# Kernel optimization log

Hardware: AMD Instinct MI355X
Metric: run time of the kernel (lower is better)

Reference implementation:

```python
import jax, jax.numpy as jnp
import numpy as np

# Config constants (from model_cfg)
X_RANGE = (0.0, 70.4)
Y_RANGE = (-40.0, 40.0)
Z_RANGE = (-3.0, 1.0)
RES = 0.2
Z_RES = 0.8
B, C, RH, RW = 2, 64, 64, 2048
W = int((Y_RANGE[1] - Y_RANGE[0]) / RES)   # 400
H = int((X_RANGE[1] - X_RANGE[0]) / RES)   # 352
D = int((Z_RANGE[1] - Z_RANGE[0]) / Z_RES) # 5


def setup_inputs() -> dict:
    key = jax.random.key(0)
    k1, k2, k3, k4 = jax.random.split(key, 4)
    range_res = jax.random.normal(k1, (B, C, RH, RW), dtype=jnp.float32)
    # realistic lidar xyz: x forward, y lateral, z height (slightly wider than
    # the crop ranges so clamping / z-dropping paths are exercised)
    x = jax.random.uniform(k2, (B, 1, RH, RW), minval=-5.0, maxval=75.0)
    y = jax.random.uniform(k3, (B, 1, RH, RW), minval=-45.0, maxval=45.0)
    z = jax.random.uniform(k4, (B, 1, RH, RW), minval=-3.5, maxval=1.5)
    rangemap_xyz = jnp.concatenate([x, y, z], axis=1).astype(jnp.float32)
    return {"range_res": range_res, "rangemap_xyz": rangemap_xyz, "batch_size": B}


def reference(range_res, rangemap_xyz, batch_size):
    b, c, rh, rw = range_res.shape
    n = rh * rw
    pts = rangemap_xyz.reshape(b, 3, n)            # [B,3,N]
    xp, yp, zp = pts[:, 0], pts[:, 1], pts[:, 2]   # [B,N] each
    feat = range_res.reshape(b, c, n).transpose(0, 2, 1)  # [B,N,C]

    # torch .long() truncates toward zero, as does astype(int32)
    x_img = (-yp / RES).astype(jnp.int32) - int(np.floor(Y_RANGE[0] / RES))
    y_img = (-xp / RES).astype(jnp.int32) + int(np.floor(X_RANGE[1] / RES))
    x_img = jnp.clip(x_img, 0, W - 1)
    y_img = jnp.clip(y_img, 0, H - 1)

    # height-bin index; points outside [z0, z1) are dropped (never scattered)
    zbin = jnp.floor((zp - Z_RANGE[0]) / Z_RES).astype(jnp.int32)
    valid = (zp >= Z_RANGE[0]) & (zp < Z_RANGE[1])
    zbin = jnp.where(valid, zbin, D)  # D is out-of-bounds -> mode='drop'

    # im is flipped along both spatial dims after the scatter; equivalent to
    # scattering at flipped indices.
    xf = (W - 1) - x_img
    yf = (H - 1) - y_img

    bidx = jnp.arange(b, dtype=jnp.int32)[:, None]  # [B,1] broadcast over N
    bev = jnp.zeros((b, D, W, H, c), dtype=range_res.dtype)
    bev = bev.at[bidx, zbin, xf, yf].set(feat, mode="drop")

    # original: bev [b,w,h,c,d] -> permute(0,3,4,1,2) = [b,c,d,w,h]
    # ours is [b,d,w,h,c] -> [b,c,d,w,h]
    return bev.transpose(0, 4, 1, 2, 3)
```

## Files before the change

### kernel.cpp

```cpp
#include <hip/hip_runtime.h>


namespace {

typedef float v4f __attribute__((ext_vector_type(4)));

constexpr int Wg    = 400;
constexpr int Hg    = 352;
constexpr int Dg    = 5;
constexpr int NCELL = Dg * Wg * Hg;
constexpr int NPTS  = 64 * 2048;
constexpr int CC    = 64;
constexpr int BB    = 2;
constexpr int CPB   = 1024;
constexpr int NCHUNK = (NCELL + CPB - 1) / CPB;

__global__ void scatter_winner_k(const float* __restrict__ xyz,
                                 int* __restrict__ winner) {
    int idx = blockIdx.x * blockDim.x + threadIdx.x;
    if (idx >= BB * NPTS) return;
    int b = idx >> 17;
    int i = idx & (NPTS - 1);
    const float* base = xyz + (size_t)b * 3 * NPTS;
    float xp = base[i];
    float yp = base[NPTS + i];
    float zp = base[2 * NPTS + i];
    if (!(zp >= -3.0f && zp < 1.0f)) return;
    int zbin  = (int)floorf((zp + 3.0f) / 0.8f);
    int x_img = (int)(-yp / 0.2f) + 200;
    int y_img = (int)(-xp / 0.2f) + 352;
    x_img = min(max(x_img, 0), Wg - 1);
    y_img = min(max(y_img, 0), Hg - 1);
    int xf = (Wg - 1) - x_img;
    int yf = (Hg - 1) - y_img;
    int cell = (zbin * Wg + xf) * Hg + yf;
    atomicMax(winner + b * NCELL + cell, i);
}

__global__ __launch_bounds__(256) void write_out_k(
        const float* __restrict__ feat,
        const int*   __restrict__ winner,
        float*       __restrict__ out) {
    int blk   = blockIdx.x;
    int b     = blk / NCHUNK;
    int chunk = blk - b * NCHUNK;
    int cell0 = chunk * CPB + (int)threadIdx.x * 4;
    if (cell0 >= NCELL) return;

    const int4 w4 = *reinterpret_cast<const int4*>(winner + b * NCELL + cell0);
    const bool v0 = w4.x >= 0, v1 = w4.y >= 0, v2 = w4.z >= 0, v3 = w4.w >= 0;
    const int  i0 = max(w4.x, 0), i1 = max(w4.y, 0);
    const int  i2 = max(w4.z, 0), i3 = max(w4.w, 0);

    const float* fb = feat + (size_t)b * CC * NPTS;
    float*       ob = out  + (size_t)b * CC * NCELL + cell0;

#pragma unroll 2
    for (int c = 0; c < CC; ++c) {
        const float* frow = fb + (size_t)c * NPTS;
        float g0 = frow[i0], g1 = frow[i1], g2 = frow[i2], g3 = frow[i3];
        v4f v;
        v.x = v0 ? g0 : 0.0f;
        v.y = v1 ? g1 : 0.0f;
        v.z = v2 ? g2 : 0.0f;
        v.w = v3 ? g3 : 0.0f;
        __builtin_nontemporal_store(v, reinterpret_cast<v4f*>(ob + (size_t)c * NCELL));
    }
}

}

extern "C" void kernel_launch(void* const* d_in, const int* in_sizes, int n_in,
                              void* d_out, int out_size, void* d_ws, size_t ws_size,
                              hipStream_t stream) {
    const float* range_res = (const float*)d_in[0];
    const float* xyz       = (const float*)d_in[1];
    float* out             = (float*)d_out;
    int* winner            = (int*)d_ws;

    (void)hipMemsetAsync(winner, 0xFF, (size_t)BB * NCELL * sizeof(int), stream);

    {
        int total = BB * NPTS;
        scatter_winner_k<<<(total + 255) / 256, 256, 0, stream>>>(xyz, winner);
    }
    {
        int blocks = BB * NCHUNK;
        write_out_k<<<blocks, 256, 0, stream>>>(range_res, winner, out);
    }
}
```

Measured before the change: 555.7 us.

## Restructure output writer to per-channel row blocks with contiguous cell streaming

The write-out kernel previously assigned each block a chunk of cells and looped over all 64 channels, gathering from 64 different feature rows. Now each block owns one (batch, channel) pair and one eighth of the cells. It re-reads winner indices and gathers from a single 512 KB feature row that can stay in cache. Block ids are interleaved so that 8 channels sharing the same winner slice run together. The cost is that the winner array is read once per channel instead of once, which adds extra winner traffic.

```diff
diff --git a/kernel.cpp b/kernel.cpp
--- a/kernel.cpp
+++ b/kernel.cpp
@@ -12,8 +12,9 @@
 constexpr int NPTS  = 64 * 2048;
 constexpr int CC    = 64;
 constexpr int BB    = 2;
-constexpr int CPB   = 1024;
-constexpr int NCHUNK = (NCELL + CPB - 1) / CPB;
+constexpr int Q     = 8;
+constexpr int CPC   = NCELL / Q;
+constexpr int VPC   = CPC / 4;
 
 __global__ void scatter_winner_k(const float* __restrict__ xyz,
                                  int* __restrict__ winner) {
@@ -41,30 +42,30 @@
         const float* __restrict__ feat,
         const int*   __restrict__ winner,
         float*       __restrict__ out) {
-    int blk   = blockIdx.x;
-    int b     = blk / NCHUNK;
-    int chunk = blk - b * NCHUNK;
-    int cell0 = chunk * CPB + (int)threadIdx.x * 4;
-    if (cell0 >= NCELL) return;
+    int blk  = blockIdx.x;
+    int x    = blk & 7;
+    int q    = (blk >> 3) & 7;
+    int bchi = blk >> 6;
+    int bc   = bchi * 8 + x;
+    int b    = bc >> 6;
 
-    const int4 w4 = *reinterpret_cast<const int4*>(winner + b * NCELL + cell0);
-    const bool v0 = w4.x >= 0, v1 = w4.y >= 0, v2 = w4.z >= 0, v3 = w4.w >= 0;
-    const int  i0 = max(w4.x, 0), i1 = max(w4.y, 0);
-    const int  i2 = max(w4.z, 0), i3 = max(w4.w, 0);
-
-    const float* fb = feat + (size_t)b * CC * NPTS;
-    float*       ob = out  + (size_t)b * CC * NCELL + cell0;
+    const int*   wbase = winner + b * NCELL + q * CPC;
+    const float* frow  = feat + (size_t)bc * NPTS;
+    float*       obase = out + (size_t)bc * NCELL + q * CPC;
 
 #pragma unroll 2
-    for (int c = 0; c < CC; ++c) {
-        const float* frow = fb + (size_t)c * NPTS;
-        float g0 = frow[i0], g1 = frow[i1], g2 = frow[i2], g3 = frow[i3];
+    for (int i = threadIdx.x; i < VPC; i += 256) {
+        const int4 w4 = reinterpret_cast<const int4*>(wbase)[i];
+        float g0 = frow[max(w4.x, 0)];
+        float g1 = frow[max(w4.y, 0)];
+        float g2 = frow[max(w4.z, 0)];
+        float g3 = frow[max(w4.w, 0)];
         v4f v;
-        v.x = v0 ? g0 : 0.0f;
-        v.y = v1 ? g1 : 0.0f;
-        v.z = v2 ? g2 : 0.0f;
-        v.w = v3 ? g3 : 0.0f;
-        __builtin_nontemporal_store(v, reinterpret_cast<v4f*>(ob + (size_t)c * NCELL));
+        v.x = (w4.x >= 0) ? g0 : 0.0f;
+        v.y = (w4.y >= 0) ? g1 : 0.0f;
+        v.z = (w4.z >= 0) ? g2 : 0.0f;
+        v.w = (w4.w >= 0) ? g3 : 0.0f;
+        __builtin_nontemporal_store(v, reinterpret_cast<v4f*>(obase) + i);
     }
 }
 
@@ -85,7 +86,7 @@
         scatter_winner_k<<<(total + 255) / 256, 256, 0, stream>>>(xyz, winner);
     }
     {
-        int blocks = BB * NCHUNK;
+        int blocks = BB * CC * Q;
         write_out_k<<<blocks, 256, 0, stream>>>(range_res, winner, out);
     }
 }
```

New measurement: 488.9 us. -12.0%, faster.

## Transpose features to point-major layout and stage BEV writes through shared memory

Applied to the files above, without the earlier changes.

Adds a pre-pass that transposes features from channel-major to point-major so each winning point's 64 channels are read contiguously. The output kernel gathers per-cell channel vectors into a shared tile, then writes channel-major output with coalesced stores. The goal is to replace 64 scattered gathers per cell with contiguous reads. In exchange it adds an extra full read and write of the feature tensor and drops the vectorized 4-wide stores.

```diff
diff --git a/kernel.cpp b/kernel.cpp
--- a/kernel.cpp
+++ b/kernel.cpp
@@ -2,8 +2,6 @@
 
 
 namespace {
-
-typedef float v4f __attribute__((ext_vector_type(4)));
 
 constexpr int Wg    = 400;
 constexpr int Hg    = 352;
@@ -12,8 +10,8 @@
 constexpr int NPTS  = 64 * 2048;
 constexpr int CC    = 64;
 constexpr int BB    = 2;
-constexpr int CPB   = 1024;
-constexpr int NCHUNK = (NCELL + CPB - 1) / CPB;
+constexpr int GRP   = 64;
+constexpr int NGRP  = NCELL / GRP;
 
 __global__ void scatter_winner_k(const float* __restrict__ xyz,
                                  int* __restrict__ winner) {
@@ -37,34 +35,62 @@
     atomicMax(winner + b * NCELL + cell, i);
 }
 
-__global__ __launch_bounds__(256) void write_out_k(
-        const float* __restrict__ feat,
-        const int*   __restrict__ winner,
-        float*       __restrict__ out) {
+__global__ __launch_bounds__(256) void transpose_k(const float* __restrict__ feat,
+                                                   float* __restrict__ featT) {
+    __shared__ float tile[64][65];
+    int blk = blockIdx.x;
+    int b   = blk >> 11;
+    int n0  = (blk & 2047) * 64;
+    const float* fb = feat  + (size_t)b * CC * NPTS;
+    float*       tb = featT + (size_t)b * NPTS * CC;
+    int t = threadIdx.x;
+#pragma unroll
+    for (int k = 0; k < 16; ++k) {
+        int j = k * 256 + t;
+        int c = j >> 6, nn = j & 63;
+        tile[c][nn] = fb[(size_t)c * NPTS + n0 + nn];
+    }
+    __syncthreads();
+#pragma unroll
+    for (int k = 0; k < 16; ++k) {
+        int j = k * 256 + t;
+        int nn = j >> 6, c = j & 63;
+        tb[(size_t)(n0 + nn) * CC + c] = tile[c][nn];
+    }
+}
+
+__global__ __launch_bounds__(256) void bev_write_k(const float* __restrict__ featT,
+                                                   const int*   __restrict__ winner,
+                                                   float*       __restrict__ out) {
+    __shared__ float tile[GRP][65];
+    __shared__ int   wins[GRP];
     int blk   = blockIdx.x;
-    int b     = blk / NCHUNK;
-    int chunk = blk - b * NCHUNK;
-    int cell0 = chunk * CPB + (int)threadIdx.x * 4;
-    if (cell0 >= NCELL) return;
+    int b     = blk / NGRP;
+    int cell0 = (blk - b * NGRP) * GRP;
+    int t     = threadIdx.x;
 
-    const int4 w4 = *reinterpret_cast<const int4*>(winner + b * NCELL + cell0);
-    const bool v0 = w4.x >= 0, v1 = w4.y >= 0, v2 = w4.z >= 0, v3 = w4.w >= 0;
-    const int  i0 = max(w4.x, 0), i1 = max(w4.y, 0);
-    const int  i2 = max(w4.z, 0), i3 = max(w4.w, 0);
+    if (t < GRP) wins[t] = winner[b * NCELL + cell0 + t];
+    __syncthreads();
 
-    const float* fb = feat + (size_t)b * CC * NPTS;
-    float*       ob = out  + (size_t)b * CC * NCELL + cell0;
-
-#pragma unroll 2
-    for (int c = 0; c < CC; ++c) {
-        const float* frow = fb + (size_t)c * NPTS;
-        float g0 = frow[i0], g1 = frow[i1], g2 = frow[i2], g3 = frow[i3];
-        v4f v;
-        v.x = v0 ? g0 : 0.0f;
-        v.y = v1 ? g1 : 0.0f;
-        v.z = v2 ? g2 : 0.0f;
-        v.w = v3 ? g3 : 0.0f;
-        __builtin_nontemporal_store(v, reinterpret_cast<v4f*>(ob + (size_t)c * NCELL));
+    const float* ftb = featT + (size_t)b * NPTS * CC;
+#pragma unroll
+    for (int k = 0; k < 16; ++k) {
+        int j = k * 256 + t;
+        int g = j >> 6;
+        int c = j & 63;
+        int pt = wins[g];
+        float v = 0.0f;
+        if (pt >= 0) v = ftb[(size_t)pt * CC + c];
+        tile[g][c] = v;
+    }
+    __syncthreads();
+    float* ob = out + (size_t)b * CC * NCELL + cell0;
+#pragma unroll
+    for (int k = 0; k < 16; ++k) {
+        int j = k * 256 + t;
+        int c = j >> 6;
+        int g = j & 63;
+        __builtin_nontemporal_store(tile[g][c], ob + (size_t)c * NCELL + g);
     }
 }
 
@@ -76,7 +102,8 @@
     const float* range_res = (const float*)d_in[0];
     const float* xyz       = (const float*)d_in[1];
     float* out             = (float*)d_out;
-    int* winner            = (int*)d_ws;
+    int*   winner          = (int*)d_ws;
+    float* featT           = (float*)((char*)d_ws + (8u << 20));
 
     (void)hipMemsetAsync(winner, 0xFF, (size_t)BB * NCELL * sizeof(int), stream);
 
@@ -85,7 +112,11 @@
         scatter_winner_k<<<(total + 255) / 256, 256, 0, stream>>>(xyz, winner);
     }
     {
-        int blocks = BB * NCHUNK;
-        write_out_k<<<blocks, 256, 0, stream>>>(range_res, winner, out);
+        int blocks = BB * (NPTS / 64);
+        transpose_k<<<blocks, 256, 0, stream>>>(range_res, featT);
+    }
+    {
+        int blocks = BB * NGRP;
+        bev_write_k<<<blocks, 256, 0, stream>>>(featT, winner, out);
     }
 }
```

New measurement: 445.9 us. 1.25x faster.
